# Optimization experiments

Measured on AMD Instinct MI355X. Metric: run time of the kernel, lower is better.

The kernel has to match this reference:

```python
import jax, jax.numpy as jnp
import numpy as np
import math

B, S, F_IN, D, H = 2048, 100, 158, 512, 8
HD = D // H  # head dim = 64


def _sinusoidal_pe(max_len, d_model):
    pos = np.arange(max_len, dtype=np.float32)[:, None]
    div = np.exp(np.arange(0, d_model, 2, dtype=np.float32) * (-math.log(10000.0) / d_model))
    pe = np.zeros((max_len, d_model), dtype=np.float32)
    pe[:, 0::2] = np.sin(pos * div)
    pe[:, 1::2] = np.cos(pos * div)
    return jnp.asarray(pe)


def setup_inputs() -> dict:
    key = jax.random.key(0)
    ks = jax.random.split(key, 16)
    s = 0.03  # small init scale to keep softmax well-conditioned
    return {
        "src": jax.random.normal(ks[0], (B, S, F_IN), jnp.float32),
        "W_feat": jax.random.normal(ks[1], (D, F_IN), jnp.float32) * s,
        "b_feat": jnp.zeros((D,), jnp.float32),
        "pe": _sinusoidal_pe(100, D),
        "Wq": jax.random.normal(ks[2], (D, D), jnp.float32) * s,
        "bq": jnp.zeros((D,), jnp.float32),
        "Wk": jax.random.normal(ks[3], (D, D), jnp.float32) * s,
        "bk": jnp.zeros((D,), jnp.float32),
        "Wv": jax.random.normal(ks[4], (D, D), jnp.float32) * s,
        "bv": jnp.zeros((D,), jnp.float32),
        "Wo": jax.random.normal(ks[5], (D, D), jnp.float32) * s,
        "bo": jnp.zeros((D,), jnp.float32),
        "ln_w": jnp.ones((D,), jnp.float32),
        "ln_b": jnp.zeros((D,), jnp.float32),
        "W1": jax.random.normal(ks[6], (F_IN, D), jnp.float32) * s,
        "b1": jnp.zeros((F_IN,), jnp.float32),
        "W2": jax.random.normal(ks[7], (D, F_IN), jnp.float32) * s,
        "b2": jnp.zeros((D,), jnp.float32),
        "Wt": jax.random.normal(ks[8], (D, D), jnp.float32) * s,
        "W_out": jax.random.normal(ks[9], (1, D), jnp.float32) * s,
        "b_out": jnp.zeros((1,), jnp.float32),
    }


def _layernorm(x, w, b, eps=1e-5):
    mu = jnp.mean(x, axis=-1, keepdims=True)
    var = jnp.var(x, axis=-1, keepdims=True)
    return (x - mu) * jax.lax.rsqrt(var + eps) * w + b


def reference(src, W_feat, b_feat, pe, Wq, bq, Wk, bk, Wv, bv, Wo, bo,
              ln_w, ln_b, W1, b1, W2, b2, Wt, W_out, b_out):
    # feature projection + sinusoidal PE  (dropout is identity in eval mode)
    x = src @ W_feat.T + b_feat            # [B,S,D]
    x = x + pe[:S]                          # [B,S,D]

    # naive multi-head attention
    def heads(t):  # [B,S,D] -> [B,H,S,HD]
        return t.reshape(B, S, H, HD).transpose(0, 2, 1, 3)
    q = heads(x @ Wq.T + bq)
    k = heads(x @ Wk.T + bk)
    v = heads(x @ Wv.T + bv)
    scores = jnp.einsum('bhqd,bhkd->bhqk', q, k) / jnp.sqrt(jnp.float32(HD))
    probs = jax.nn.softmax(scores, axis=-1)
    attn = jnp.einsum('bhqk,bhkd->bhqd', probs, v)
    attn = attn.transpose(0, 2, 1, 3).reshape(B, S, D)
    attn_out = attn @ Wo.T + bo

    # addnorm #1: x + LayerNorm(x) (note: residual is of the SAME tensor)
    y1 = attn_out + _layernorm(attn_out, ln_w, ln_b)

    # FFN (hidden = 158 per the code's d_ff reuse)
    ffn = jax.nn.relu(y1 @ W1.T + b1) @ W2.T + b2

    # addnorm #2 (same shared AddNormLayer params)
    y2 = ffn + _layernorm(ffn, ln_w, ln_b)

    # temporal attention pooling over time
    h = y2 @ Wt.T                           # [B,S,D]
    lam = jnp.einsum('bsd,bd->bs', h, h[:, -1, :])
    lam = jax.nn.softmax(lam, axis=1)
    pooled = jnp.einsum('bs,bsd->bd', lam, y2)  # [B,D]

    return pooled @ W_out.T + b_out         # [B,1]
```

## Files before the change

kernel.cpp:

```cpp
#include <hip/hip_runtime.h>
#include <math.h>

#define NB 2048
#define NS 100
#define NF 158
#define ND 512
#define NH 8

typedef unsigned short u16;
typedef __attribute__((ext_vector_type(8))) short bf16x8;
typedef __attribute__((ext_vector_type(8))) unsigned short u16x8;
typedef __attribute__((ext_vector_type(4))) float f32x4;

__device__ __forceinline__ u16 f2bf(float f) {
    union { float f; unsigned u; } v; v.f = f;
    unsigned u = v.u;
    return (u16)((u + 0x7fffu + ((u >> 16) & 1u)) >> 16);
}

__device__ __forceinline__ void gload16(const void* g, void* l) {
    __builtin_amdgcn_global_load_lds(
        (const __attribute__((address_space(1))) unsigned*)g,
        (__attribute__((address_space(3))) unsigned*)l, 16, 0, 0);
}

__device__ __forceinline__ bf16x8 load8_cvt(const float* __restrict__ base, int c0) {
    bf16x8 r;
    if (c0 + 8 <= NF) {
        #pragma unroll
        for (int j = 0; j < 8; j += 2) {
            float2 v = *(const float2*)(base + c0 + j);
            r[j] = (short)f2bf(v.x); r[j + 1] = (short)f2bf(v.y);
        }
    } else {
        #pragma unroll
        for (int j = 0; j < 8; ++j)
            r[j] = (c0 + j < NF) ? (short)f2bf(base[c0 + j]) : (short)0;
    }
    return r;
}

__global__ __launch_bounds__(256) void prep_w_kernel(
    const float* __restrict__ Wq, const float* __restrict__ Wk,
    const float* __restrict__ Wv, const float* __restrict__ Wfeat,
    u16* __restrict__ Wf)
{
    int bid = blockIdx.x;
    int sel = bid >> 9;
    int n = bid & 511;
    const float* Wsrc = (sel == 0) ? Wq : (sel == 1) ? Wk : Wv;
    __shared__ float wrow[ND];
    int t = threadIdx.x;
    wrow[t] = Wsrc[(size_t)n * ND + t];
    wrow[t + 256] = Wsrc[(size_t)n * ND + t + 256];
    __syncthreads();
    if (t < 160) {
        float acc = 0.f;
        if (t < NF)
            for (int d = 0; d < ND; ++d)
                acc += wrow[d] * Wfeat[(size_t)d * NF + t];
        int h = n >> 6, ni = (n >> 4) & 3, l16 = n & 15;
        int ks = t >> 5, quad = (t >> 3) & 3, j = t & 7;
        size_t idx = (((((size_t)sel * 8 + h) * 4 + ni) * 5 + ks) * 64
                      + (quad << 4) + l16) * 8 + j;
        Wf[idx] = f2bf(acc);
    }
}

__global__ __launch_bounds__(256) void prep_c_kernel(
    const float* __restrict__ Wq, const float* __restrict__ Wk, const float* __restrict__ Wv,
    const float* __restrict__ bq, const float* __restrict__ bk, const float* __restrict__ bv,
    const float* __restrict__ bfeat, const float* __restrict__ pe,
    float* __restrict__ T4)
{
    int bid = blockIdx.x;
    int sel = bid / 100;
    int s = bid - sel * 100;
    const float* Wsrc = (sel == 0) ? Wq : (sel == 1) ? Wk : Wv;
    const float* bsrc = (sel == 0) ? bq : (sel == 1) ? bk : bv;
    __shared__ float xv[ND];
    int t = threadIdx.x;
    xv[t] = bfeat[t] + pe[(size_t)s * ND + t];
    xv[t + 256] = bfeat[t + 256] + pe[(size_t)s * ND + t + 256];
    __syncthreads();
    #pragma unroll
    for (int rr = 0; rr < 2; ++rr) {
        int r = t + (rr << 8);
        const float* wr = Wsrc + (size_t)r * ND;
        float acc = bsrc[r];
        for (int d = 0; d < ND; d += 4) {
            float4 w4 = *(const float4*)(wr + d);
            acc += w4.x * xv[d] + w4.y * xv[d+1] + w4.z * xv[d+2] + w4.w * xv[d+3];
        }
        int h = r >> 6, ni = (r >> 4) & 3, l16 = r & 15;
        T4[(((size_t)(sel * 8 + h)) * 100 + s) * 64 + (l16 << 2) + ni] = acc;
    }
}

__global__ __launch_bounds__(256) void pad_cast_kernel(
    const float* __restrict__ src, u16* __restrict__ dst,
    int R, int C, int Cp, int total)
{
    int idx = blockIdx.x * 256 + threadIdx.x;
    if (idx >= total) return;
    int r = idx / Cp, c = idx - r * Cp;
    float v = (r < R && c < C) ? src[(size_t)r * C + c] : 0.f;
    dst[idx] = f2bf(v);
}

__global__ __launch_bounds__(256) void pad_b1_kernel(
    const float* __restrict__ b1, float* __restrict__ b1p)
{
    int t = threadIdx.x;
    b1p[t] = (t < NF) ? b1[t] : 0.f;
}

#define ALDQ 72
#define ALDP 136

__global__ __launch_bounds__(512, 4) void qkv_attn_kernel(
    const float* __restrict__ src, const u16* __restrict__ Wf,
    const float* __restrict__ T4, u16* __restrict__ O)
{
    __shared__ short UN[128 * ALDP];
    __shared__ short Ks[112 * ALDQ];
    __shared__ short Vt[64 * ALDP];

    int t = threadIdx.x;
    int lane = t & 63, wave = t >> 6;
    int quad = lane >> 4, l16 = lane & 15;
    int rows0 = wave << 4;
    int b = blockIdx.x;
    const float* xb = src + (size_t)b * NS * NF;
    const size_t rowbase = (size_t)b * NS;
    f32x4 z = {0.f, 0.f, 0.f, 0.f};

    for (int l = t; l < 12 * ALDQ; l += 512)
        Ks[(100 + l / ALDQ) * ALDQ + (l % ALDQ)] = 0;
    for (int l = t; l < 64 * 28; l += 512) {
        int d = l / 28, s = 100 + (l - d * 28);
        Vt[d * ALDP + s] = 0;
    }

    int arow = rows0 + l16;
    bf16x8 AF[5];
    {
        const float* xr = xb + (size_t)arow * NF;
        #pragma unroll
        for (int ks = 0; ks < 5; ++ks) {
            if (arow < NS) AF[ks] = load8_cvt(xr, (ks << 5) + (quad << 3));
            else { bf16x8 zz = {0,0,0,0,0,0,0,0}; AF[ks] = zz; }
        }
    }

    for (int h = 0; h < NH; ++h) {
        #pragma unroll
        for (int sel = 0; sel < 3; ++sel) {
            f32x4 acc[4];
            #pragma unroll
            for (int ni = 0; ni < 4; ++ni) acc[ni] = z;
            #pragma unroll
            for (int ks = 0; ks < 5; ++ks) {
                bf16x8 wfr[4];
                #pragma unroll
                for (int ni = 0; ni < 4; ++ni)
                    wfr[ni] = *(const bf16x8*)(Wf +
                        (((((size_t)sel * 8 + h) * 4 + ni) * 5 + ks) * 64 + lane) * 8);
                #pragma unroll
                for (int ni = 0; ni < 4; ++ni)
                    acc[ni] = __builtin_amdgcn_mfma_f32_16x16x32_bf16(
                        AF[ks], wfr[ni], acc[ni], 0, 0, 0);
            }
            #pragma unroll
            for (int r = 0; r < 4; ++r) {
                int row_s = rows0 + (quad << 2) + r;
                bool real = row_s < NS;
                float4 tv = make_float4(0.f, 0.f, 0.f, 0.f);
                if (real)
                    tv = *(const float4*)(T4 +
                        (((size_t)(sel * 8 + h)) * 100 + row_s) * 64 + (l16 << 2));
                float tvs[4] = {tv.x, tv.y, tv.z, tv.w};
                #pragma unroll
                for (int ni = 0; ni < 4; ++ni) {
                    int nloc = (ni << 4) + l16;
                    float v = acc[ni][r] + tvs[ni];
                    u16 bv = f2bf(v);
                    if (sel == 0) UN[row_s * ALDP + nloc] = (short)bv;
                    else if (sel == 1) { if (real) Ks[row_s * ALDQ + nloc] = (short)bv; }
                    else               { if (real) Vt[nloc * ALDP + row_s] = (short)bv; }
                }
            }
        }
        __syncthreads();

        f32x4 sc[7];
        #pragma unroll
        for (int ni = 0; ni < 7; ++ni) sc[ni] = z;
        #pragma unroll
        for (int ks = 0; ks < 2; ++ks) {
            bf16x8 aq = *(const bf16x8*)&UN[(rows0 + l16) * ALDP + (ks << 5) + (quad << 3)];
            bf16x8 bk[7];
            #pragma unroll
            for (int ni = 0; ni < 7; ++ni)
                bk[ni] = *(const bf16x8*)&Ks[((ni << 4) + l16) * ALDQ + (ks << 5) + (quad << 3)];
            #pragma unroll
            for (int ni = 0; ni < 7; ++ni)
                sc[ni] = __builtin_amdgcn_mfma_f32_16x16x32_bf16(aq, bk[ni], sc[ni], 0, 0, 0);
        }
        __syncthreads();

        #pragma unroll
        for (int r = 0; r < 4; ++r) {
            if (l16 >= 4) sc[6][r] = -3.0e38f;
            float mx = sc[0][r];
            #pragma unroll
            for (int ni = 1; ni < 7; ++ni) mx = fmaxf(mx, sc[ni][r]);
            #pragma unroll
            for (int off = 1; off < 16; off <<= 1) mx = fmaxf(mx, __shfl_xor(mx, off));
            float sum = 0.f;
            #pragma unroll
            for (int ni = 0; ni < 7; ++ni) {
                float e = expf((sc[ni][r] - mx) * 0.125f);
                sc[ni][r] = e; sum += e;
            }
            #pragma unroll
            for (int off = 1; off < 16; off <<= 1) sum += __shfl_xor(sum, off);
            float inv = 1.f / sum;
            int row = rows0 + (quad << 2) + r;
            #pragma unroll
            for (int ni = 0; ni < 7; ++ni)
                UN[row * ALDP + (ni << 4) + l16] = (short)f2bf(sc[ni][r] * inv);
            UN[row * ALDP + 112 + l16] = 0;
        }
        __syncthreads();

        f32x4 oa[4];
        #pragma unroll
        for (int ni = 0; ni < 4; ++ni) oa[ni] = z;
        #pragma unroll
        for (int ks = 0; ks < 4; ++ks) {
            bf16x8 ap = *(const bf16x8*)&UN[(rows0 + l16) * ALDP + (ks << 5) + (quad << 3)];
            bf16x8 bv[4];
            #pragma unroll
            for (int ni = 0; ni < 4; ++ni)
                bv[ni] = *(const bf16x8*)&Vt[((ni << 4) + l16) * ALDP + (ks << 5) + (quad << 3)];
            #pragma unroll
            for (int ni = 0; ni < 4; ++ni)
                oa[ni] = __builtin_amdgcn_mfma_f32_16x16x32_bf16(ap, bv[ni], oa[ni], 0, 0, 0);
        }
        #pragma unroll
        for (int r = 0; r < 4; ++r) {
            int row = rows0 + (quad << 2) + r;
            if (row < NS) {
                u16* orow = O + (rowbase + row) * 512 + (h << 6);
                #pragma unroll
                for (int ni = 0; ni < 4; ++ni)
                    orow[(ni << 4) + l16] = f2bf(oa[ni][r]);
            }
        }
        __syncthreads();
    }
}

template<int OUTMODE, bool RELU>
__global__ __launch_bounds__(256) void gemm_bf16(
    const u16* __restrict__ A, const u16* __restrict__ W,
    const float* __restrict__ bias, void* __restrict__ Cv, int K, int ldc)
{
    __shared__ short As[128 * 32];
    __shared__ short Bs[128 * 32];
    int t = threadIdx.x;
    int lane = t & 63, wave = t >> 6;
    int quad = lane >> 4, l16 = lane & 15;
    int wr = wave >> 1, wc = wave & 1;
    int m0 = blockIdx.y << 7, n0 = blockIdx.x << 7;

    f32x4 acc[4][4];
    f32x4 z = {0.f, 0.f, 0.f, 0.f};
    #pragma unroll
    for (int mi = 0; mi < 4; ++mi)
        #pragma unroll
        for (int ni = 0; ni < 4; ++ni) acc[mi][ni] = z;

    int rowA = t >> 2;
    int cch = (t & 3) << 3;
    const u16* aSrc0 = A + (size_t)(m0 + rowA) * K + cch;
    const u16* aSrc1 = A + (size_t)(m0 + rowA + 64) * K + cch;
    const u16* bSrc0 = W + (size_t)(n0 + rowA) * K + cch;
    const u16* bSrc1 = W + (size_t)(n0 + rowA + 64) * K + cch;
    short* aDst0 = As + t * 8;
    short* aDst1 = As + (t + 256) * 8;
    short* bDst0 = Bs + t * 8;
    short* bDst1 = Bs + (t + 256) * 8;

    int nk = K >> 5;
    for (int kc = 0; kc < nk; ++kc) {
        if (kc) __syncthreads();
        gload16(aSrc0, aDst0);
        gload16(aSrc1, aDst1);
        gload16(bSrc0, bDst0);
        gload16(bSrc1, bDst1);
        aSrc0 += 32; aSrc1 += 32; bSrc0 += 32; bSrc1 += 32;
        __syncthreads();

        bf16x8 af[4], bw[4];
        #pragma unroll
        for (int mi = 0; mi < 4; ++mi)
            af[mi] = *(const bf16x8*)(As + ((size_t)((wr << 6) + (mi << 4) + l16) * 32 + (quad << 3)));
        #pragma unroll
        for (int ni = 0; ni < 4; ++ni)
            bw[ni] = *(const bf16x8*)(Bs + ((size_t)((wc << 6) + (ni << 4) + l16) * 32 + (quad << 3)));
        #pragma unroll
        for (int mi = 0; mi < 4; ++mi)
            #pragma unroll
            for (int ni = 0; ni < 4; ++ni)
                acc[mi][ni] = __builtin_amdgcn_mfma_f32_16x16x32_bf16(af[mi], bw[ni], acc[mi][ni], 0, 0, 0);
    }

    #pragma unroll
    for (int mi = 0; mi < 4; ++mi) {
        #pragma unroll
        for (int r = 0; r < 4; ++r) {
            int row = m0 + (wr << 6) + (mi << 4) + (quad << 2) + r;
            #pragma unroll
            for (int ni = 0; ni < 4; ++ni) {
                int col = n0 + (wc << 6) + (ni << 4) + l16;
                float v = acc[mi][ni][r];
                if (bias) v += bias[col];
                if (RELU) v = fmaxf(v, 0.f);
                if (OUTMODE == 0)
                    ((float*)Cv)[(size_t)row * ldc + col] = v;
                else
                    ((u16*)Cv)[(size_t)row * ldc + col] = f2bf(v);
            }
        }
    }
}

template<int OUTMODE>
__global__ __launch_bounds__(512, 2) void gemm_ln(
    const u16* __restrict__ A, const u16* __restrict__ W,
    const float* __restrict__ bias, const float* __restrict__ lnw,
    const float* __restrict__ lnb, void* __restrict__ outv, int K)
{
    __shared__ short As[64 * 32];
    __shared__ short Bs[512 * 32];
    __shared__ float red_s[64][9];
    __shared__ float red_q[64][9];
    __shared__ float mrow[64], rrow[64];

    int t = threadIdx.x;
    int lane = t & 63, wave = t >> 6;
    int quad = lane >> 4, l16 = lane & 15;
    int m0 = blockIdx.x << 6;

    f32x4 acc[4][4];
    f32x4 z = {0.f, 0.f, 0.f, 0.f};
    #pragma unroll
    for (int mi = 0; mi < 4; ++mi)
        #pragma unroll
        for (int ni = 0; ni < 4; ++ni) acc[mi][ni] = z;

    int koff = (t & 3) << 3;
    const u16* aSrc = A + (size_t)(m0 + (t >> 2)) * K + koff;
    const u16* bSrc0 = W + (size_t)(t >> 2) * K + koff;
    const u16* bSrc1 = W + (size_t)((t >> 2) + 128) * K + koff;
    const u16* bSrc2 = W + (size_t)((t >> 2) + 256) * K + koff;
    const u16* bSrc3 = W + (size_t)((t >> 2) + 384) * K + koff;
    short* aDst = As + t * 8;
    short* bDst0 = Bs + t * 8;
    short* bDst1 = Bs + (t + 512) * 8;
    short* bDst2 = Bs + (t + 1024) * 8;
    short* bDst3 = Bs + (t + 1536) * 8;

    int nk = K >> 5;
    for (int kc = 0; kc < nk; ++kc) {
        if (kc) __syncthreads();
        if (t < 256) gload16(aSrc, aDst);
        gload16(bSrc0, bDst0);
        gload16(bSrc1, bDst1);
        gload16(bSrc2, bDst2);
        gload16(bSrc3, bDst3);
        aSrc += 32; bSrc0 += 32; bSrc1 += 32; bSrc2 += 32; bSrc3 += 32;
        __syncthreads();

        bf16x8 af[4], bw[4];
        #pragma unroll
        for (int mi = 0; mi < 4; ++mi)
            af[mi] = *(const bf16x8*)(As + ((mi << 4) + l16) * 32 + (quad << 3));
        #pragma unroll
        for (int ni = 0; ni < 4; ++ni)
            bw[ni] = *(const bf16x8*)(Bs + ((wave << 6) + (ni << 4) + l16) * 32 + (quad << 3));
        #pragma unroll
        for (int mi = 0; mi < 4; ++mi)
            #pragma unroll
            for (int ni = 0; ni < 4; ++ni)
                acc[mi][ni] = __builtin_amdgcn_mfma_f32_16x16x32_bf16(af[mi], bw[ni], acc[mi][ni], 0, 0, 0);
    }

    float lwv[4], lbv[4];
    #pragma unroll
    for (int ni = 0; ni < 4; ++ni) {
        int col = (wave << 6) + (ni << 4) + l16;
        float bv = bias[col];
        lwv[ni] = lnw[col];
        lbv[ni] = lnb[col];
        #pragma unroll
        for (int mi = 0; mi < 4; ++mi)
            #pragma unroll
            for (int r = 0; r < 4; ++r) acc[mi][ni][r] += bv;
    }
    #pragma unroll
    for (int mi = 0; mi < 4; ++mi) {
        #pragma unroll
        for (int r = 0; r < 4; ++r) {
            float s = acc[mi][0][r] + acc[mi][1][r] + acc[mi][2][r] + acc[mi][3][r];
            float q = acc[mi][0][r]*acc[mi][0][r] + acc[mi][1][r]*acc[mi][1][r]
                    + acc[mi][2][r]*acc[mi][2][r] + acc[mi][3][r]*acc[mi][3][r];
            #pragma unroll
            for (int off = 1; off < 16; off <<= 1) {
                s += __shfl_xor(s, off);
                q += __shfl_xor(q, off);
            }
            if (l16 == 0) {
                int row = (mi << 4) + (quad << 2) + r;
                red_s[row][wave] = s;
                red_q[row][wave] = q;
            }
        }
    }
    __syncthreads();
    if (t < 64) {
        float s = 0.f, q = 0.f;
        #pragma unroll
        for (int w8 = 0; w8 < 8; ++w8) { s += red_s[t][w8]; q += red_q[t][w8]; }
        float mean = s * (1.f / 512.f);
        float var = q * (1.f / 512.f) - mean * mean;
        mrow[t] = mean;
        rrow[t] = rsqrtf(var + 1e-5f);
    }
    __syncthreads();
    #pragma unroll
    for (int mi = 0; mi < 4; ++mi) {
        #pragma unroll
        for (int r = 0; r < 4; ++r) {
            int lrow = (mi << 4) + (quad << 2) + r;
            float mean = mrow[lrow], rstd = rrow[lrow];
            size_t grow = (size_t)(m0 + lrow) * 512;
            #pragma unroll
            for (int ni = 0; ni < 4; ++ni) {
                int col = (wave << 6) + (ni << 4) + l16;
                float v = acc[mi][ni][r];
                float y = v + (v - mean) * rstd * lwv[ni] + lbv[ni];
                if (OUTMODE == 0) ((float*)outv)[grow + col] = y;
                else ((u16*)outv)[grow + col] = f2bf(y);
            }
        }
    }
}

__global__ __launch_bounds__(256) void u_stage1_kernel(
    const float* __restrict__ Y2, const float* __restrict__ Wt,
    float* __restrict__ T1)
{
    __shared__ float yl[16][512];
    int t = threadIdx.x;
    int r0 = blockIdx.x << 6;
    int bg = blockIdx.y << 4;
    for (int l = t; l < 2048; l += 256) {
        int bb = l >> 7, seg = (l & 127) << 2;
        *(float4*)&yl[bb][seg] =
            *(const float4*)&Y2[((size_t)(bg + bb) * NS + 99) * ND + seg];
    }
    __syncthreads();
    int r = r0 + (t & 63);
    int b0 = t >> 6;
    const float* wr = Wt + (size_t)r * ND;
    float acc[4] = {0.f, 0.f, 0.f, 0.f};
    for (int d = 0; d < ND; d += 4) {
        float4 w4 = *(const float4*)(wr + d);
        #pragma unroll
        for (int bb = 0; bb < 4; ++bb) {
            int bl = (b0 << 2) + bb;
            acc[bb] += w4.x * yl[bl][d] + w4.y * yl[bl][d+1]
                     + w4.z * yl[bl][d+2] + w4.w * yl[bl][d+3];
        }
    }
    #pragma unroll
    for (int bb = 0; bb < 4; ++bb)
        T1[(size_t)(bg + (b0 << 2) + bb) * ND + r] = acc[bb];
}

__global__ __launch_bounds__(256) void u_stage2_kernel(
    const float* __restrict__ T1, const float* __restrict__ Wt,
    float* __restrict__ U)
{
    __shared__ float t1s[16][512];
    int t = threadIdx.x;
    int c0 = blockIdx.x << 6;
    int bg = blockIdx.y << 4;
    for (int l = t; l < 2048; l += 256) {
        int bb = l >> 7, seg = (l & 127) << 2;
        *(float4*)&t1s[bb][seg] = *(const float4*)&T1[(size_t)(bg + bb) * ND + seg];
    }
    __syncthreads();
    int c = c0 + (t & 63);
    int b0 = t >> 6;
    float acc[4] = {0.f, 0.f, 0.f, 0.f};
    for (int r = 0; r < ND; ++r) {
        float w = Wt[(size_t)r * ND + c];
        #pragma unroll
        for (int bb = 0; bb < 4; ++bb)
            acc[bb] += w * t1s[(b0 << 2) + bb][r];
    }
    #pragma unroll
    for (int bb = 0; bb < 4; ++bb)
        U[(size_t)(bg + (b0 << 2) + bb) * ND + c] = acc[bb];
}

__global__ __launch_bounds__(256) void pool_kernel(
    const float* __restrict__ Y2, const float* __restrict__ U,
    const float* __restrict__ Wout, const float* __restrict__ bout,
    float* __restrict__ out)
{
    __shared__ float u[ND];
    __shared__ float lam[128];
    __shared__ float red[4];
    int t = threadIdx.x;
    int b = blockIdx.x;
    const float* y2b = Y2 + (size_t)b * NS * ND;
    u[t] = U[(size_t)b * ND + t];
    u[t + 256] = U[(size_t)b * ND + t + 256];
    __syncthreads();
    int wid = t >> 6, lane = t & 63;
    int c0 = lane << 2;
    for (int s = wid; s < NS; s += 4) {
        const float* yr = y2b + (size_t)s * ND;
        float4 p0 = *(const float4*)(yr + c0);
        float4 p1 = *(const float4*)(yr + 256 + c0);
        float a = p0.x*u[c0] + p0.y*u[c0+1] + p0.z*u[c0+2] + p0.w*u[c0+3]
                + p1.x*u[256+c0] + p1.y*u[256+c0+1] + p1.z*u[256+c0+2] + p1.w*u[256+c0+3];
        #pragma unroll
        for (int off = 32; off > 0; off >>= 1) a += __shfl_xor(a, off);
        if (lane == 0) lam[s] = a;
    }
    __syncthreads();
    if (t < 64) {
        float l0 = lam[t];
        float l1 = (t + 64 < NS) ? lam[t + 64] : -3.0e38f;
        float mx = fmaxf(l0, l1);
        #pragma unroll
        for (int off = 32; off > 0; off >>= 1) mx = fmaxf(mx, __shfl_xor(mx, off));
        float e0 = expf(l0 - mx);
        float e1 = (t + 64 < NS) ? expf(l1 - mx) : 0.f;
        float ssum = e0 + e1;
        #pragma unroll
        for (int off = 32; off > 0; off >>= 1) ssum += __shfl_xor(ssum, off);
        float inv = 1.f / ssum;
        lam[t] = e0 * inv;
        if (t + 64 < NS) lam[t + 64] = e1 * inv;
    }
    __syncthreads();
    float p0 = 0.f, p1 = 0.f;
    for (int s = 0; s < NS; ++s) {
        float lm = lam[s];
        const float* yr = y2b + (size_t)s * ND;
        p0 += lm * yr[t];
        p1 += lm * yr[t + 256];
    }
    float vd = p0 * Wout[t] + p1 * Wout[t + 256];
    #pragma unroll
    for (int off = 32; off > 0; off >>= 1) vd += __shfl_xor(vd, off);
    if (lane == 0) red[wid] = vd;
    __syncthreads();
    if (t == 0) out[b] = red[0] + red[1] + red[2] + red[3] + bout[0];
}

static size_t ws_need(int CBc) {
    size_t cm = (size_t)CBc * NS;
    size_t b = 0;
    b += cm * 512 * 2;
    b += cm * 512 * 2;
    b += cm * 256 * 2;
    b += cm * 512 * 4;
    b += (size_t)CBc * 512 * 4 * 2;
    b += 1536 * 160 * 2;
    b += 512 * 512 * 2 + 256 * 512 * 2 + 512 * 256 * 2;
    b += 3 * 8 * 100 * 64 * 4;
    b += 256 * 4;
    b += 64 * 1024;
    return b;
}

extern "C" void kernel_launch(void* const* d_in, const int* in_sizes, int n_in,
                              void* d_out, int out_size, void* d_ws, size_t ws_size,
                              hipStream_t stream)
{
    const float* src   = (const float*)d_in[0];
    const float* Wfeat = (const float*)d_in[1];
    const float* bfeat = (const float*)d_in[2];
    const float* pe    = (const float*)d_in[3];
    const float* Wq    = (const float*)d_in[4];
    const float* bq    = (const float*)d_in[5];
    const float* Wk    = (const float*)d_in[6];
    const float* bk    = (const float*)d_in[7];
    const float* Wv    = (const float*)d_in[8];
    const float* bv    = (const float*)d_in[9];
    const float* Wo    = (const float*)d_in[10];
    const float* bo    = (const float*)d_in[11];
    const float* lnw   = (const float*)d_in[12];
    const float* lnb   = (const float*)d_in[13];
    const float* W1    = (const float*)d_in[14];
    const float* b1    = (const float*)d_in[15];
    const float* W2    = (const float*)d_in[16];
    const float* b2    = (const float*)d_in[17];
    const float* Wt    = (const float*)d_in[18];
    const float* Wout  = (const float*)d_in[19];
    const float* bout  = (const float*)d_in[20];
    float* out = (float*)d_out;

    int CBc = (ws_size >= ws_need(1024)) ? 1024
            : (ws_size >= ws_need(512))  ? 512
            : (ws_size >= ws_need(256))  ? 256 : 128;
    int NCH = NB / CBc;
    size_t CMc = (size_t)CBc * NS;

    char* p = (char*)d_ws;
    auto alloc = [&](size_t bytes) { char* r = p; p += (bytes + 255) & ~(size_t)255; return r; };
    u16*   AO16  = (u16*)  alloc(CMc * 512 * 2);
    u16*   Y116  = (u16*)  alloc(CMc * 512 * 2);
    u16*   ACT16 = (u16*)  alloc(CMc * 256 * 2);
    float* Y2    = (float*)alloc(CMc * 512 * 4);
    float* T1    = (float*)alloc((size_t)CBc * 512 * 4);
    float* U     = (float*)alloc((size_t)CBc * 512 * 4);
    u16*   Wf    = (u16*)  alloc(1536 * 160 * 2);
    u16*   Wo16  = (u16*)  alloc(512 * 512 * 2);
    u16*   W116  = (u16*)  alloc(256 * 512 * 2);
    u16*   W216  = (u16*)  alloc(512 * 256 * 2);
    float* T4    = (float*)alloc(3 * 8 * 100 * 64 * 4);
    float* b1p   = (float*)alloc(256 * 4);

    prep_w_kernel<<<1536, 256, 0, stream>>>(Wq, Wk, Wv, Wfeat, Wf);
    prep_c_kernel<<<300, 256, 0, stream>>>(Wq, Wk, Wv, bq, bk, bv, bfeat, pe, T4);
    pad_cast_kernel<<<(512 * 512) / 256, 256, 0, stream>>>(Wo, Wo16, 512, 512, 512, 512 * 512);
    pad_cast_kernel<<<(256 * 512) / 256, 256, 0, stream>>>(W1, W116, NF, 512, 512, 256 * 512);
    pad_cast_kernel<<<(512 * 256) / 256, 256, 0, stream>>>(W2, W216, 512, NF, 256, 512 * 256);
    pad_b1_kernel<<<1, 256, 0, stream>>>(b1, b1p);

    dim3 g256(2, CMc / 128);
    dim3 gU(8, CBc / 16);
    int gLN = CMc / 64;

    for (int c = 0; c < NCH; ++c) {
        const float* srcC = src + (size_t)c * CMc * NF;
        float* outC = out + (size_t)c * CBc;

        qkv_attn_kernel<<<CBc, 512, 0, stream>>>(srcC, Wf, T4, AO16);
        gemm_ln<1><<<gLN, 512, 0, stream>>>(AO16, Wo16, bo, lnw, lnb, Y116, 512);
        gemm_bf16<1, true><<<g256, 256, 0, stream>>>(Y116, W116, b1p, ACT16, 512, 256);
        gemm_ln<0><<<gLN, 512, 0, stream>>>(ACT16, W216, b2, lnw, lnb, Y2, 256);
        u_stage1_kernel<<<gU, 256, 0, stream>>>(Y2, Wt, T1);
        u_stage2_kernel<<<gU, 256, 0, stream>>>(T1, Wt, U);
        pool_kernel<<<CBc, 256, 0, stream>>>(Y2, U, Wout, bout, outC);
    }

    (void)in_sizes; (void)n_in; (void)out_size; (void)ws_size;
}
```

Before: 1.552 ms.

## Store Y2 in bf16 and permute Q/K columns for packed LDS stores

The second add-norm output Y2 is now written as bf16 instead of fp32, halving its write and the reads made by the u_stage1 and pool kernels. The Q and K weight columns and the bias table T4 are permuted so each lane holds four adjacent columns, letting the QKV epilogue write one packed 8-byte LDS store per row instead of four scalar stores. The permutation is applied consistently to Q and K, so their dot products are unchanged. The trade is lower precision in Y2, which feeds the temporal pooling softmax.

```diff
diff --git a/kernel.cpp b/kernel.cpp
--- a/kernel.cpp
+++ b/kernel.cpp
@@ -18,6 +18,10 @@
     return (u16)((u + 0x7fffu + ((u >> 16) & 1u)) >> 16);
 }
 
+__device__ __forceinline__ float bf2f(u16 v) {
+    union { unsigned u; float f; } x; x.u = ((unsigned)v) << 16; return x.f;
+}
+
 __device__ __forceinline__ void gload16(const void* g, void* l) {
     __builtin_amdgcn_global_load_lds(
         (const __attribute__((address_space(1))) unsigned*)g,
@@ -59,7 +63,10 @@
         if (t < NF)
             for (int d = 0; d < ND; ++d)
                 acc += wrow[d] * Wfeat[(size_t)d * NF + t];
-        int h = n >> 6, ni = (n >> 4) & 3, l16 = n & 15;
+        int h = n >> 6, local = n & 63;
+        int ni, l16;
+        if (sel < 2) { ni = local & 3; l16 = local >> 2; }
+        else         { ni = (local >> 4) & 3; l16 = local & 15; }
         int ks = t >> 5, quad = (t >> 3) & 3, j = t & 7;
         size_t idx = (((((size_t)sel * 8 + h) * 4 + ni) * 5 + ks) * 64
                       + (quad << 4) + l16) * 8 + j;
@@ -92,8 +99,9 @@
             float4 w4 = *(const float4*)(wr + d);
             acc += w4.x * xv[d] + w4.y * xv[d+1] + w4.z * xv[d+2] + w4.w * xv[d+3];
         }
-        int h = r >> 6, ni = (r >> 4) & 3, l16 = r & 15;
-        T4[(((size_t)(sel * 8 + h)) * 100 + s) * 64 + (l16 << 2) + ni] = acc;
+        int h = r >> 6, local = r & 63;
+        int idx64 = (sel < 2) ? local : (((local & 15) << 2) | (local >> 4));
+        T4[(((size_t)(sel * 8 + h)) * 100 + s) * 64 + idx64] = acc;
     }
 }
 
@@ -179,15 +187,22 @@
                 if (real)
                     tv = *(const float4*)(T4 +
                         (((size_t)(sel * 8 + h)) * 100 + row_s) * 64 + (l16 << 2));
-                float tvs[4] = {tv.x, tv.y, tv.z, tv.w};
-                #pragma unroll
-                for (int ni = 0; ni < 4; ++ni) {
-                    int nloc = (ni << 4) + l16;
-                    float v = acc[ni][r] + tvs[ni];
-                    u16 bv = f2bf(v);
-                    if (sel == 0) UN[row_s * ALDP + nloc] = (short)bv;
-                    else if (sel == 1) { if (real) Ks[row_s * ALDQ + nloc] = (short)bv; }
-                    else               { if (real) Vt[nloc * ALDP + row_s] = (short)bv; }
+                if (sel < 2) {
+                    ushort4 pk;
+                    pk.x = f2bf(acc[0][r] + tv.x);
+                    pk.y = f2bf(acc[1][r] + tv.y);
+                    pk.z = f2bf(acc[2][r] + tv.z);
+                    pk.w = f2bf(acc[3][r] + tv.w);
+                    if (sel == 0) *(ushort4*)&UN[row_s * ALDP + (l16 << 2)] = pk;
+                    else if (real) *(ushort4*)&Ks[row_s * ALDQ + (l16 << 2)] = pk;
+                } else {
+                    float tvs[4] = {tv.x, tv.y, tv.z, tv.w};
+                    #pragma unroll
+                    for (int ni = 0; ni < 4; ++ni) {
+                        int nloc = (ni << 4) + l16;
+                        float v = acc[ni][r] + tvs[ni];
+                        if (real) Vt[nloc * ALDP + row_s] = (short)f2bf(v);
+                    }
                 }
             }
         }
@@ -460,17 +475,18 @@
 }
 
 __global__ __launch_bounds__(256) void u_stage1_kernel(
-    const float* __restrict__ Y2, const float* __restrict__ Wt,
+    const u16* __restrict__ Y2, const float* __restrict__ Wt,
     float* __restrict__ T1)
 {
     __shared__ float yl[16][512];
     int t = threadIdx.x;
     int r0 = blockIdx.x << 6;
     int bg = blockIdx.y << 4;
-    for (int l = t; l < 2048; l += 256) {
-        int bb = l >> 7, seg = (l & 127) << 2;
-        *(float4*)&yl[bb][seg] =
-            *(const float4*)&Y2[((size_t)(bg + bb) * NS + 99) * ND + seg];
+    for (int l = t; l < 1024; l += 256) {
+        int bb = l >> 6, seg = (l & 63) << 3;
+        u16x8 v = *(const u16x8*)&Y2[((size_t)(bg + bb) * NS + 99) * ND + seg];
+        #pragma unroll
+        for (int j = 0; j < 8; ++j) yl[bb][seg + j] = bf2f(v[j]);
     }
     __syncthreads();
     int r = r0 + (t & 63);
@@ -519,7 +535,7 @@
 }
 
 __global__ __launch_bounds__(256) void pool_kernel(
-    const float* __restrict__ Y2, const float* __restrict__ U,
+    const u16* __restrict__ Y2, const float* __restrict__ U,
     const float* __restrict__ Wout, const float* __restrict__ bout,
     float* __restrict__ out)
 {
@@ -528,18 +544,19 @@
     __shared__ float red[4];
     int t = threadIdx.x;
     int b = blockIdx.x;
-    const float* y2b = Y2 + (size_t)b * NS * ND;
+    const u16* y2b = Y2 + (size_t)b * NS * ND;
     u[t] = U[(size_t)b * ND + t];
     u[t + 256] = U[(size_t)b * ND + t + 256];
     __syncthreads();
     int wid = t >> 6, lane = t & 63;
     int c0 = lane << 2;
     for (int s = wid; s < NS; s += 4) {
-        const float* yr = y2b + (size_t)s * ND;
-        float4 p0 = *(const float4*)(yr + c0);
-        float4 p1 = *(const float4*)(yr + 256 + c0);
-        float a = p0.x*u[c0] + p0.y*u[c0+1] + p0.z*u[c0+2] + p0.w*u[c0+3]
-                + p1.x*u[256+c0] + p1.y*u[256+c0+1] + p1.z*u[256+c0+2] + p1.w*u[256+c0+3];
+        const u16* yr = y2b + (size_t)s * ND;
+        ushort4 q0 = *(const ushort4*)(yr + c0);
+        ushort4 q1 = *(const ushort4*)(yr + 256 + c0);
+        float a = bf2f(q0.x)*u[c0] + bf2f(q0.y)*u[c0+1] + bf2f(q0.z)*u[c0+2] + bf2f(q0.w)*u[c0+3]
+                + bf2f(q1.x)*u[256+c0] + bf2f(q1.y)*u[256+c0+1]
+                + bf2f(q1.z)*u[256+c0+2] + bf2f(q1.w)*u[256+c0+3];
         #pragma unroll
         for (int off = 32; off > 0; off >>= 1) a += __shfl_xor(a, off);
         if (lane == 0) lam[s] = a;
@@ -564,9 +581,9 @@
     float p0 = 0.f, p1 = 0.f;
     for (int s = 0; s < NS; ++s) {
         float lm = lam[s];
-        const float* yr = y2b + (size_t)s * ND;
-        p0 += lm * yr[t];
-        p1 += lm * yr[t + 256];
+        const u16* yr = y2b + (size_t)s * ND;
+        p0 += lm * bf2f(yr[t]);
+        p1 += lm * bf2f(yr[t + 256]);
     }
     float vd = p0 * Wout[t] + p1 * Wout[t + 256];
     #pragma unroll
@@ -582,7 +599,7 @@
     b += cm * 512 * 2;
     b += cm * 512 * 2;
     b += cm * 256 * 2;
-    b += cm * 512 * 4;
+    b += cm * 512 * 2;
     b += (size_t)CBc * 512 * 4 * 2;
     b += 1536 * 160 * 2;
     b += 512 * 512 * 2 + 256 * 512 * 2 + 512 * 256 * 2;
@@ -630,7 +647,7 @@
     u16*   AO16  = (u16*)  alloc(CMc * 512 * 2);
     u16*   Y116  = (u16*)  alloc(CMc * 512 * 2);
     u16*   ACT16 = (u16*)  alloc(CMc * 256 * 2);
-    float* Y2    = (float*)alloc(CMc * 512 * 4);
+    u16*   Y2    = (u16*)  alloc(CMc * 512 * 2);
     float* T1    = (float*)alloc((size_t)CBc * 512 * 4);
     float* U     = (float*)alloc((size_t)CBc * 512 * 4);
     u16*   Wf    = (u16*)  alloc(1536 * 160 * 2);
@@ -658,7 +675,7 @@
         qkv_attn_kernel<<<CBc, 512, 0, stream>>>(srcC, Wf, T4, AO16);
         gemm_ln<1><<<gLN, 512, 0, stream>>>(AO16, Wo16, bo, lnw, lnb, Y116, 512);
         gemm_bf16<1, true><<<g256, 256, 0, stream>>>(Y116, W116, b1p, ACT16, 512, 256);
-        gemm_ln<0><<<gLN, 512, 0, stream>>>(ACT16, W216, b2, lnw, lnb, Y2, 256);
+        gemm_ln<1><<<gLN, 512, 0, stream>>>(ACT16, W216, b2, lnw, lnb, Y2, 256);
         u_stage1_kernel<<<gU, 256, 0, stream>>>(Y2, Wt, T1);
         u_stage2_kernel<<<gU, 256, 0, stream>>>(T1, Wt, U);
         pool_kernel<<<CBc, 256, 0, stream>>>(Y2, U, Wout, bout, outC);
```

Result: faster. 1.484 ms (-4.4%).
